# Performance work log

Hardware: AMD Instinct MI355X
Metric: run time of the kernel (lower is better)

Reference implementation:

```python
import jax, jax.numpy as jnp
import numpy as np
import math

N, E = 50000, 800000
DM, H, L = 128, 8, 6
D = DM // H  # per-head dim = 16
FF = 4 * DM
EPS = 1e-5


def _ln(x, g, b):
    mu = jnp.mean(x, axis=-1, keepdims=True)
    var = jnp.mean((x - mu) ** 2, axis=-1, keepdims=True)
    return (x - mu) * jax.lax.rsqrt(var + EPS) * g + b


def setup_inputs() -> dict:
    key = jax.random.key(0)
    ks = jax.random.split(key, 20)
    s = 0.05
    inp = {
        "node_features": jax.random.normal(ks[0], (N, 20), jnp.float32),
        "edge_attr": jax.random.normal(ks[1], (E, 3), jnp.float32),
        "edge_index": jax.random.randint(ks[2], (2, E), 0, N, jnp.int32),
        "emb_W": jax.random.normal(ks[3], (20, DM), jnp.float32) * s,
        "emb_b": jnp.zeros((DM,), jnp.float32),
        "Wq": jax.random.normal(ks[4], (L, DM, DM), jnp.float32) * s,
        "Wk": jax.random.normal(ks[5], (L, DM, DM), jnp.float32) * s,
        "Wv": jax.random.normal(ks[6], (L, DM, DM), jnp.float32) * s,
        "eW1": jax.random.normal(ks[7], (L, 3, D), jnp.float32) * s,
        "eb1": jnp.zeros((L, D), jnp.float32),
        "eW2": jax.random.normal(ks[8], (L, D, DM), jnp.float32) * s,
        "eb2": jnp.zeros((L, DM), jnp.float32),
        "ln_g": jnp.ones((L, DM), jnp.float32),
        "ln_b": jnp.zeros((L, DM), jnp.float32),
        "ff_W1": jax.random.normal(ks[9], (L, DM, FF), jnp.float32) * s,
        "ff_b1": jnp.zeros((L, FF), jnp.float32),
        "ff_W2": jax.random.normal(ks[10], (L, FF, DM), jnp.float32) * s,
        "ff_b2": jnp.zeros((L, DM), jnp.float32),
    }
    return inp


def reference(node_features, edge_attr, emb_W, emb_b, Wq, Wk, Wv,
              eW1, eb1, eW2, eb2, ln_g, ln_b, ff_W1, ff_b1, ff_W2, ff_b2,
              edge_index):
    src = edge_index[0]  # j: message source
    dst = edge_index[1]  # i: message target
    x = node_features @ emb_W + emb_b  # [N, DM]
    scale = 1.0 / math.sqrt(D)
    for l in range(L):
        q = (x @ Wq[l]).reshape(N, H, D)
        k = (x @ Wk[l]).reshape(N, H, D)
        v = (x @ Wv[l]).reshape(N, H, D)
        ee = (jnp.maximum(edge_attr @ eW1[l] + eb1[l], 0.0) @ eW2[l] + eb2[l]).reshape(E, H, D)
        # per-edge attention logits over heads (softmax over head axis, as in source)
        attn = jnp.einsum('ehd,ehd->eh', q[dst], k[src] + ee) * scale
        attn = jax.nn.softmax(attn, axis=1)  # [E, H]
        msg = (attn[..., None] * v[src]).reshape(E, H * D)  # per-head messages, concat heads
        agg = jax.ops.segment_sum(msg, dst, num_segments=N)  # scatter-add
        x = _ln(x + agg, ln_g[l], ln_b[l])
        h = jnp.maximum(x @ ff_W1[l] + ff_b1[l], 0.0) @ ff_W2[l] + ff_b2[l]
        x = _ln(x + h, ln_g[l], ln_b[l])  # same LN params reused, as in source
    return x
```

## Files before the change

kernel.cpp:

```cpp
#include <hip/hip_runtime.h>
#include <cstdint>
#include <cstddef>

#define NN 50000
#define NE 800000
#define NP 50048
#define ROWT 391

typedef unsigned short u16;
typedef _Float16 f16;
typedef _Float16 hf8 __attribute__((ext_vector_type(8)));
typedef float f32x4 __attribute__((ext_vector_type(4)));

union U32 { unsigned u; f16 h[2]; };
union U64 { uint2 v; f16 h[4]; };
union U128 { uint4 v; f16 x[8]; };

__device__ __forceinline__ float b2f(u16 v){ return __uint_as_float((unsigned)v << 16); }
__device__ __forceinline__ u16 f2b(float f){
  unsigned u = __float_as_uint(f);
  return (u16)((u + 0x7fffu + ((u >> 16) & 1u)) >> 16);
}
__device__ __forceinline__ float ldf(const void* p, long i, int f32){
  return f32 ? ((const float*)p)[i] : b2f(((const u16*)p)[i]);
}
__device__ __forceinline__ void gl_lds16(const void* g, void* l){
  __builtin_amdgcn_global_load_lds((const __attribute__((address_space(1))) void*)g,
                                   (__attribute__((address_space(3))) void*)l, 16, 0, 0);
}

__global__ void detect_k(const u16* __restrict__ nf, int* __restrict__ flag)
{
  int mx = 0;
  for (int i = 0; i < 256; ++i) { int e = (nf[i] >> 7) & 0xFF; mx = e > mx ? e : mx; }
  flag[0] = (mx >= 0x90) ? 1 : 0;
}

__global__ void zero_i_k(int* __restrict__ p, int n)
{
  int i = blockIdx.x * 256 + threadIdx.x;
  if (i < n) p[i] = 0;
}

__global__ void conv_k(const void* eW1, const void* eb1, const void* eb2,
                       const void* lng, const void* lnb, const void* fb1, const void* fb2,
                       const void* embB, const void* embW,
                       float* __restrict__ pf, const int* __restrict__ dflag)
{
  int f32 = dflag[0];
  int i = blockIdx.x * 256 + threadIdx.x;
  if (i >= 9216) return;
  const void* p; long off;
  if (i < 288)       { p = eW1;  off = i; }
  else if (i < 384)  { p = eb1;  off = i - 288; }
  else if (i < 1152) { p = eb2;  off = i - 384; }
  else if (i < 1920) { p = lng;  off = i - 1152; }
  else if (i < 2688) { p = lnb;  off = i - 1920; }
  else if (i < 5760) { p = fb1;  off = i - 2688; }
  else if (i < 6528) { p = fb2;  off = i - 5760; }
  else if (i < 6656) { p = embB; off = i - 6528; }
  else               { p = embW; off = i - 6656; }
  pf[i] = ldf(p, off, f32);
}

__global__ void prep_qkve_k(const void* __restrict__ Wq, const void* __restrict__ Wk,
                            const void* __restrict__ Wv, const void* __restrict__ eW2,
                            f16* __restrict__ Wcat, const int* __restrict__ dflag)
{
  int f32 = dflag[0];
  int idx = blockIdx.x * 256 + threadIdx.x;
  int l = idx >> 16;
  int rem = idx & 65535;
  int r = rem >> 7;
  int kk = rem & 127;
  long base = (long)l * 16384;
  float val;
  if (r < 384) {
    const void* W = (r < 128) ? Wq : (r < 256) ? Wk : Wv;
    int n = r & 127;
    val = ldf(W, base + kk * 128 + n, f32);
  } else {
    int n = r - 384, h = n >> 4, j = n & 15;
    long wq = base + kk * 128 + h * 16;
    long e2 = (long)l * 2048 + j * 128 + h * 16;
    float s = 0.f;
    #pragma unroll
    for (int d = 0; d < 16; ++d) s += ldf(Wq, wq + d, f32) * ldf(eW2, e2 + d, f32);
    val = s;
  }
  Wcat[idx] = (f16)val;
}

__global__ void transpose_k(const void* __restrict__ in, f16* __restrict__ out, int R, int C,
                            const int* __restrict__ dflag)
{
  int f32 = dflag[0];
  int idx = blockIdx.x * 256 + threadIdx.x;
  int rc = R * C;
  int l = idx / rc, rem = idx % rc;
  int r = rem / C, c = rem % C;
  out[l * rc + c * R + r] = (f16)ldf(in, idx, f32);
}

__global__ void deg_count_k(const int* __restrict__ eidx, int* __restrict__ deg)
{
  int e = blockIdx.x * 256 + threadIdx.x;
  if (e < NE) atomicAdd(&deg[eidx[NE + e]], 1);
}

__global__ void scan_k(const int* __restrict__ deg, int* __restrict__ rstart,
                       int* __restrict__ cursor, int Nn)
{
  __shared__ int sums[1024];
  int t = threadIdx.x;
  int chunk = (Nn + 1023) >> 10;
  int start = t * chunk;
  int end = start + chunk; if (end > Nn) end = Nn;
  int s = 0;
  for (int i = start; i < end; ++i) s += deg[i];
  sums[t] = s;
  __syncthreads();
  for (int o = 1; o < 1024; o <<= 1) {
    int v = (t >= o) ? sums[t - o] : 0;
    __syncthreads();
    sums[t] += v;
    __syncthreads();
  }
  int run = (t == 0) ? 0 : sums[t - 1];
  for (int i = start; i < end; ++i) { rstart[i] = run; cursor[i] = run; run += deg[i]; }
  if (end == Nn && start < Nn) rstart[Nn] = run;
}

__global__ void csr_fill_k(const int* __restrict__ eidx, int* __restrict__ cursor,
                           int* __restrict__ csrc, int* __restrict__ cdst,
                           int* __restrict__ ceid)
{
  int e = blockIdx.x * 256 + threadIdx.x;
  if (e >= NE) return;
  int d = eidx[NE + e];
  int slot = atomicAdd(&cursor[d], 1);
  csrc[slot] = eidx[e];
  cdst[slot] = d;
  ceid[slot] = e;
}

__global__ void ea_gather_k(const void* __restrict__ eatt, const int* __restrict__ ceid,
                            f16* __restrict__ ea4, const int* __restrict__ dflag)
{
  int f32 = dflag[0];
  int e = blockIdx.x * 256 + threadIdx.x;
  if (e >= NE) return;
  long id = ceid[e];
  f16* q = ea4 + (size_t)e * 4;
  q[0] = (f16)ldf(eatt, id * 3 + 0, f32);
  q[1] = (f16)ldf(eatt, id * 3 + 1, f32);
  q[2] = (f16)ldf(eatt, id * 3 + 2, f32);
  q[3] = (f16)0.f;
}

__global__ void emb_k(const void* __restrict__ nf, const float* __restrict__ embWf,
                      const float* __restrict__ embBf, float* __restrict__ xf,
                      f16* __restrict__ xh, const int* __restrict__ dflag)
{
  int f32 = dflag[0];
  int idx = blockIdx.x * 256 + threadIdx.x;
  int node = idx >> 7, c = idx & 127;
  float s = 0.f;
  if (node < NN) {
    s = embBf[c];
    long row = (long)node * 20;
    #pragma unroll
    for (int f = 0; f < 20; ++f) s += ldf(nf, row + f, f32) * embWf[f * 128 + c];
  }
  xf[idx] = s;
  xh[idx] = (f16)s;
}

template<int MODE>
__global__ __launch_bounds__(256)
void gemm_k(const f16* __restrict__ A, const f16* __restrict__ Bt, int K,
            f16* __restrict__ o0, f16* __restrict__ o1, f16* __restrict__ o3,
            const float* __restrict__ bias)
{
  __shared__ __align__(16) f16 lA[128 * 32];
  __shared__ __align__(16) f16 lB[128 * 32];
  const int tid = threadIdx.x;
  const int wave = tid >> 6, lane = tid & 63;
  const int wr = wave >> 1, wc = wave & 1;
  const size_t rowBase = (size_t)blockIdx.x * 128;
  const size_t colBase = (size_t)blockIdx.y * 128;
  const int m = lane & 15, q4 = lane >> 4;

  f32x4 zero = {0.f, 0.f, 0.f, 0.f};
  f32x4 acc[4][4];
  #pragma unroll
  for (int i = 0; i < 4; ++i)
    #pragma unroll
    for (int j = 0; j < 4; ++j) acc[i][j] = zero;

  const int lr = lane >> 2, lq = lane & 3;
  const f16* Ap = A + (rowBase + wave * 32 + lr) * (size_t)K + lq * 8;
  const f16* Bp = Bt + (colBase + wave * 32 + lr) * (size_t)K + lq * 8;
  f16* lAp = lA + wave * 1024;
  f16* lBp = lB + wave * 1024;

  for (int k0 = 0; k0 < K; k0 += 32) {
    gl_lds16(Ap + k0, lAp);
    gl_lds16(Ap + k0 + (size_t)16 * K, lAp + 512);
    gl_lds16(Bp + k0, lBp);
    gl_lds16(Bp + k0 + (size_t)16 * K, lBp + 512);
    __syncthreads();
    hf8 af[4], bf[4];
    #pragma unroll
    for (int i = 0; i < 4; ++i) af[i] = *(const hf8*)(lA + (wr * 64 + i * 16 + m) * 32 + q4 * 8);
    #pragma unroll
    for (int j = 0; j < 4; ++j) bf[j] = *(const hf8*)(lB + (wc * 64 + j * 16 + m) * 32 + q4 * 8);
    #pragma unroll
    for (int i = 0; i < 4; ++i)
      #pragma unroll
      for (int j = 0; j < 4; ++j)
        acc[i][j] = __builtin_amdgcn_mfma_f32_16x16x32_f16(af[i], bf[j], acc[i][j], 0, 0, 0);
    __syncthreads();
  }

  if (MODE == 0) {
    f16* o; size_t ld; int off;
    if (blockIdx.y == 0)      { o = o0; ld = 128; off = 0; }
    else if (blockIdx.y == 1) { o = o1; ld = 256; off = 0; }
    else if (blockIdx.y == 2) { o = o1; ld = 256; off = 128; }
    else                      { o = o3; ld = 128; off = 0; }
    #pragma unroll
    for (int i = 0; i < 4; ++i)
      #pragma unroll
      for (int r = 0; r < 4; ++r) {
        size_t row = rowBase + wr * 64 + i * 16 + q4 * 4 + r;
        #pragma unroll
        for (int j = 0; j < 4; ++j) {
          int col = wc * 64 + j * 16 + m;
          o[row * ld + off + col] = (f16)acc[i][j][r];
        }
      }
  } else if (MODE == 1) {
    #pragma unroll
    for (int j = 0; j < 4; ++j) {
      int colg = (int)colBase + wc * 64 + j * 16 + m;
      float bv = bias[colg];
      #pragma unroll
      for (int i = 0; i < 4; ++i)
        #pragma unroll
        for (int r = 0; r < 4; ++r) {
          size_t row = rowBase + wr * 64 + i * 16 + q4 * 4 + r;
          o0[row * 512 + colg] = (f16)fmaxf(acc[i][j][r] + bv, 0.f);
        }
    }
  } else {
    #pragma unroll
    for (int j = 0; j < 4; ++j) {
      int colg = wc * 64 + j * 16 + m;
      float bv = bias[colg];
      #pragma unroll
      for (int i = 0; i < 4; ++i)
        #pragma unroll
        for (int r = 0; r < 4; ++r) {
          size_t row = rowBase + wr * 64 + i * 16 + q4 * 4 + r;
          o0[row * 128 + colg] = (f16)(acc[i][j][r] + bv);
        }
    }
  }
}

__global__ void pb_k(const f16* __restrict__ qf, const float* __restrict__ eb2f,
                     float* __restrict__ pbt)
{
  int idx = blockIdx.x * 256 + threadIdx.x;
  if (idx >= NN * 8) return;
  int n = idx >> 3, h = idx & 7;
  U128 a, b;
  a.v = *(const uint4*)(qf + (size_t)n * 128 + h * 16);
  b.v = *(const uint4*)(qf + (size_t)n * 128 + h * 16 + 8);
  const float* e = eb2f + h * 16;
  float p = 0.f;
  #pragma unroll
  for (int d = 0; d < 8; ++d) p = fmaf((float)a.x[d], e[d], fmaf((float)b.x[d], e[8 + d], p));
  pbt[idx] = p;
}

__global__ __launch_bounds__(256)
void attn_k(const f16* __restrict__ qf, const f16* __restrict__ kv, const f16* __restrict__ qef,
            const f16* __restrict__ ea4, const int* __restrict__ csrc, const int* __restrict__ cdst,
            const float* __restrict__ pbt, const float* __restrict__ eW1f,
            const float* __restrict__ eb1f, f16* __restrict__ w8)
{
  int e = blockIdx.x * 256 + threadIdx.x;
  if (e >= NE) return;
  int src = csrc[e], dst = cdst[e];
  U64 ue; ue.v = *(const uint2*)(ea4 + (size_t)e * 4);
  float a0 = (float)ue.h[0], a1 = (float)ue.h[1], a2 = (float)ue.h[2];
  float he[16];
  #pragma unroll
  for (int j = 0; j < 16; ++j)
    he[j] = fmaxf(fmaf(a2, eW1f[32 + j], fmaf(a1, eW1f[16 + j], fmaf(a0, eW1f[j], eb1f[j]))), 0.f);
  const uint4* qr = (const uint4*)(qf + (size_t)dst * 128);
  const uint4* kr = (const uint4*)(kv + (size_t)src * 256);
  const uint4* er = (const uint4*)(qef + (size_t)dst * 128);
  float4 pb0 = *(const float4*)(pbt + (size_t)dst * 8);
  float4 pb1 = *(const float4*)(pbt + (size_t)dst * 8 + 4);
  float pbv[8] = { pb0.x, pb0.y, pb0.z, pb0.w, pb1.x, pb1.y, pb1.z, pb1.w };
  float logit[8];
  uint4 qa = qr[0], qb = qr[1], ka = kr[0], kb = kr[1], za = er[0], zb = er[1];
  #pragma unroll
  for (int h = 0; h < 8; ++h) {
    uint4 qa2, qb2, ka2, kb2, za2, zb2;
    if (h < 7) {
      qa2 = qr[2*h+2]; qb2 = qr[2*h+3];
      ka2 = kr[2*h+2]; kb2 = kr[2*h+3];
      za2 = er[2*h+2]; zb2 = er[2*h+3];
    }
    U128 Q0, Q1, K0, K1, E0, E1;
    Q0.v = qa; Q1.v = qb; K0.v = ka; K1.v = kb; E0.v = za; E1.v = zb;
    float p = 0.f;
    #pragma unroll
    for (int d = 0; d < 8; ++d) {
      p = fmaf((float)Q0.x[d], (float)K0.x[d], p);
      p = fmaf((float)Q1.x[d], (float)K1.x[d], p);
      p = fmaf((float)E0.x[d], he[d], p);
      p = fmaf((float)E1.x[d], he[8 + d], p);
    }
    logit[h] = (p + pbv[h]) * 0.25f;
    qa = qa2; qb = qb2; ka = ka2; kb = kb2; za = za2; zb = zb2;
  }
  float mx = logit[0];
  #pragma unroll
  for (int h = 1; h < 8; ++h) mx = fmaxf(mx, logit[h]);
  float se = 0.f, ex[8];
  #pragma unroll
  for (int h = 0; h < 8; ++h) { ex[h] = __expf(logit[h] - mx); se += ex[h]; }
  float inv = 1.f / se;
  U128 W;
  #pragma unroll
  for (int h = 0; h < 8; ++h) W.x[h] = (f16)(ex[h] * inv);
  *(uint4*)(w8 + (size_t)e * 8) = W.v;
}

__global__ void agg_k(const f16* __restrict__ kv, const f16* __restrict__ w8,
                      const int* __restrict__ rstart, const int* __restrict__ csrc,
                      const float* __restrict__ gf, const float* __restrict__ bpf,
                      float* __restrict__ xf, f16* __restrict__ xh)
{
  int wave = threadIdx.x >> 6, lane = threadIdx.x & 63;
  int node = blockIdx.x * 4 + wave;
  if (node >= NN) return;
  int sub = lane >> 4, l = lane & 15;
  int c0 = l << 3;
  int head = l >> 1;
  float acc[8] = {0.f, 0.f, 0.f, 0.f, 0.f, 0.f, 0.f, 0.f};
  int e0 = rstart[node], e1 = rstart[node + 1];
  int e = e0 + sub;
  uint4 vN = {0, 0, 0, 0}; float wN = 0.f;
  if (e < e1) {
    int s = csrc[e];
    vN = *(const uint4*)(kv + (size_t)s * 256 + 128 + c0);
    wN = (float)w8[(size_t)e * 8 + head];
  }
  for (; e < e1; e += 4) {
    uint4 vC = vN; float wC = wN;
    int en = e + 4;
    if (en < e1) {
      int s = csrc[en];
      vN = *(const uint4*)(kv + (size_t)s * 256 + 128 + c0);
      wN = (float)w8[(size_t)en * 8 + head];
    }
    U128 V; V.v = vC;
    #pragma unroll
    for (int i = 0; i < 8; ++i) acc[i] = fmaf(wC, (float)V.x[i], acc[i]);
  }
  #pragma unroll
  for (int i = 0; i < 8; ++i) {
    acc[i] += __shfl_xor(acc[i], 16);
    acc[i] += __shfl_xor(acc[i], 32);
  }
  size_t nb = (size_t)node * 128 + c0;
  float4 x0 = *(const float4*)(xf + nb);
  float4 x1 = *(const float4*)(xf + nb + 4);
  float y[8] = { x0.x + acc[0], x0.y + acc[1], x0.z + acc[2], x0.w + acc[3],
                 x1.x + acc[4], x1.y + acc[5], x1.z + acc[6], x1.w + acc[7] };
  float s1 = 0.f, s2 = 0.f;
  #pragma unroll
  for (int i = 0; i < 8; ++i) { s1 += y[i]; s2 += y[i] * y[i]; }
  #pragma unroll
  for (int o = 1; o < 16; o <<= 1) { s1 += __shfl_xor(s1, o); s2 += __shfl_xor(s2, o); }
  float mu = s1 * 0.0078125f;
  float var = s2 * 0.0078125f - mu * mu;
  float rstd = rsqrtf(var + 1e-5f);
  float ov[8];
  #pragma unroll
  for (int i = 0; i < 8; ++i) ov[i] = (y[i] - mu) * rstd * gf[c0 + i] + bpf[c0 + i];
  if (sub == 0) {
    float4 s0 = { ov[0], ov[1], ov[2], ov[3] };
    float4 s1v = { ov[4], ov[5], ov[6], ov[7] };
    *(float4*)(xf + nb) = s0;
    *(float4*)(xf + nb + 4) = s1v;
    U128 wz;
    #pragma unroll
    for (int i = 0; i < 8; ++i) wz.x[i] = (f16)ov[i];
    *(uint4*)(xh + nb) = wz.v;
  }
}

__global__ void ln_res_k(const f16* __restrict__ add, float* __restrict__ xf,
                         f16* __restrict__ xh, const float* __restrict__ gf,
                         const float* __restrict__ bpf)
{
  int wave = threadIdx.x >> 6, lane = threadIdx.x & 63;
  int node = blockIdx.x * 4 + wave;
  if (node >= NN) return;
  int c0 = lane << 1;
  size_t nb = (size_t)node * 128 + c0;
  U32 ua; ua.u = *(const unsigned*)(add + nb);
  float y0 = xf[nb] + (float)ua.h[0];
  float y1 = xf[nb + 1] + (float)ua.h[1];
  float s1 = y0 + y1, s2 = y0 * y0 + y1 * y1;
  #pragma unroll
  for (int o = 1; o < 64; o <<= 1) { s1 += __shfl_xor(s1, o); s2 += __shfl_xor(s2, o); }
  float mu = s1 * 0.0078125f;
  float var = s2 * 0.0078125f - mu * mu;
  float rstd = rsqrtf(var + 1e-5f);
  float o0v = (y0 - mu) * rstd * gf[c0] + bpf[c0];
  float o1v = (y1 - mu) * rstd * gf[c0 + 1] + bpf[c0 + 1];
  xf[nb] = o0v; xf[nb + 1] = o1v;
  U32 wz; wz.h[0] = (f16)o0v; wz.h[1] = (f16)o1v;
  *(unsigned*)(xh + nb) = wz.u;
}

__global__ void out_k(const float* __restrict__ xf, void* __restrict__ out,
                      const int* __restrict__ dflag)
{
  int f32 = dflag[0];
  int idx = blockIdx.x * 256 + threadIdx.x;
  if (f32) ((float*)out)[idx] = xf[idx];
  else     ((u16*)out)[idx] = f2b(xf[idx]);
}

extern "C" void kernel_launch(void* const* d_in, const int* in_sizes, int n_in,
                              void* d_out, int out_size, void* d_ws, size_t ws_size,
                              hipStream_t stream)
{
  const void* nf   = d_in[0];
  const void* eatt = d_in[1];
  const int*  eidx = (const int*)d_in[2];
  const void* embW = d_in[3];
  const void* embB = d_in[4];
  const void* Wq   = d_in[5];
  const void* Wk   = d_in[6];
  const void* Wv   = d_in[7];
  const void* eW1  = d_in[8];
  const void* eb1  = d_in[9];
  const void* eW2  = d_in[10];
  const void* eb2  = d_in[11];
  const void* lng  = d_in[12];
  const void* lnb  = d_in[13];
  const void* fW1  = d_in[14];
  const void* fb1  = d_in[15];
  const void* fW2  = d_in[16];
  const void* fb2  = d_in[17];

  char* p = (char*)d_ws;
  auto alloc = [&](size_t b) { char* r = p; p += (b + 255) & ~(size_t)255; return r; };
  int* dflag   = (int*)alloc(256);
  float* pf    = (float*)alloc(9216 * 4);
  float* xf    = (float*)alloc((size_t)NP * 128 * 4);
  f16*   xh    = (f16*)  alloc((size_t)NP * 128 * 2);
  int* deg     = (int*)alloc((NN + 1) * 4);
  int* rst     = (int*)alloc((NN + 1) * 4);
  int* cur     = (int*)alloc((size_t)NN * 4);
  int* csrc    = (int*)alloc((size_t)NE * 4);
  int* cdst    = (int*)alloc((size_t)NE * 4);
  float* pbt   = (float*)alloc((size_t)NN * 8 * 4);
  f16* ea4     = (f16*)alloc((size_t)NE * 4 * 2);
  f16* Wcat    = (f16*)alloc((size_t)6 * 512 * 128 * 2);
  f16* W1t     = (f16*)alloc((size_t)6 * 512 * 128 * 2);
  f16* W2t     = (f16*)alloc((size_t)6 * 128 * 512 * 2);
  char* S    = alloc((size_t)NP * 512 * 2 + (size_t)NP * 128 * 2);
  f16* qf  = (f16*)S;
  f16* qe  = qf + (size_t)NP * 128;
  f16* kv  = qe + (size_t)NP * 128;
  f16* hb  = (f16*)S;
  f16* ffh = hb + (size_t)NP * 512;
  f16* w8  = ffh;
  int* ceid = (int*)S;

  float* eW1f = pf;
  float* eb1f = pf + 288;
  float* eb2f = pf + 384;
  float* lngf = pf + 1152;
  float* lnbf = pf + 1920;
  float* fb1f = pf + 2688;
  float* fb2f = pf + 5760;
  float* embBf = pf + 6528;
  float* embWf = pf + 6656;

  detect_k<<<1, 1, 0, stream>>>((const u16*)nf, dflag);
  conv_k<<<36, 256, 0, stream>>>(eW1, eb1, eb2, lng, lnb, fb1, fb2, embB, embW, pf, dflag);
  prep_qkve_k<<<1536, 256, 0, stream>>>(Wq, Wk, Wv, eW2, Wcat, dflag);
  transpose_k<<<1536, 256, 0, stream>>>(fW1, W1t, 128, 512, dflag);
  transpose_k<<<1536, 256, 0, stream>>>(fW2, W2t, 512, 128, dflag);
  zero_i_k<<<(NN + 256) / 256, 256, 0, stream>>>(deg, NN + 1);
  deg_count_k<<<3125, 256, 0, stream>>>(eidx, deg);
  scan_k<<<1, 1024, 0, stream>>>(deg, rst, cur, NN);
  csr_fill_k<<<3125, 256, 0, stream>>>(eidx, cur, csrc, cdst, ceid);
  ea_gather_k<<<3125, 256, 0, stream>>>(eatt, ceid, ea4, dflag);
  emb_k<<<NP * 128 / 256, 256, 0, stream>>>(nf, embWf, embBf, xf, xh, dflag);

  for (int l = 0; l < 6; ++l) {
    gemm_k<0><<<dim3(ROWT, 4), 256, 0, stream>>>(xh, Wcat + (size_t)l * 65536, 128,
                                                 qf, kv, qe, nullptr);
    pb_k<<<(NN * 8 + 255) / 256, 256, 0, stream>>>(qf, eb2f + l * 128, pbt);
    attn_k<<<3125, 256, 0, stream>>>(qf, kv, qe, ea4, csrc, cdst, pbt,
                                     eW1f + l * 48, eb1f + l * 16, w8);
    agg_k<<<12500, 256, 0, stream>>>(kv, w8, rst, csrc,
                                     lngf + l * 128, lnbf + l * 128, xf, xh);
    gemm_k<1><<<dim3(ROWT, 4), 256, 0, stream>>>(xh, W1t + (size_t)l * 65536, 128,
                                                 hb, nullptr, nullptr, fb1f + l * 512);
    gemm_k<2><<<dim3(ROWT, 1), 256, 0, stream>>>(hb, W2t + (size_t)l * 65536, 512,
                                                 ffh, nullptr, nullptr, fb2f + l * 128);
    ln_res_k<<<12500, 256, 0, stream>>>(ffh, xf, xh, lngf + l * 128, lnbf + l * 128);
  }
  out_k<<<25000, 256, 0, stream>>>(xf, d_out, dflag);
}
```

Before: 1.517 ms.

## Parallelize degree prefix scan across blocks and deepen GEMM K-tile to 64

```diff
diff --git a/kernel.cpp b/kernel.cpp
--- a/kernel.cpp
+++ b/kernel.cpp
@@ -6,6 +6,7 @@
 #define NE 800000
 #define NP 50048
 #define ROWT 391
+#define NBLK 196
 
 typedef unsigned short u16;
 typedef _Float16 f16;
@@ -108,27 +109,48 @@
   if (e < NE) atomicAdd(&deg[eidx[NE + e]], 1);
 }
 
-__global__ void scan_k(const int* __restrict__ deg, int* __restrict__ rstart,
-                       int* __restrict__ cursor, int Nn)
-{
-  __shared__ int sums[1024];
+__global__ void scan_a(const int* __restrict__ deg, int* __restrict__ bsum)
+{
+  __shared__ int tmp[256];
+  int t = threadIdx.x, i = blockIdx.x * 256 + t;
+  int v = (i < NN) ? deg[i] : 0;
+  tmp[t] = v; __syncthreads();
+  for (int o = 1; o < 256; o <<= 1) {
+    int u = (t >= o) ? tmp[t - o] : 0;
+    __syncthreads(); tmp[t] += u; __syncthreads();
+  }
+  if (t == 255) bsum[blockIdx.x] = tmp[255];
+}
+
+__global__ void scan_b(const int* __restrict__ bsum, int* __restrict__ boff)
+{
+  __shared__ int tmp[256];
   int t = threadIdx.x;
-  int chunk = (Nn + 1023) >> 10;
-  int start = t * chunk;
-  int end = start + chunk; if (end > Nn) end = Nn;
-  int s = 0;
-  for (int i = start; i < end; ++i) s += deg[i];
-  sums[t] = s;
-  __syncthreads();
-  for (int o = 1; o < 1024; o <<= 1) {
-    int v = (t >= o) ? sums[t - o] : 0;
-    __syncthreads();
-    sums[t] += v;
-    __syncthreads();
-  }
-  int run = (t == 0) ? 0 : sums[t - 1];
-  for (int i = start; i < end; ++i) { rstart[i] = run; cursor[i] = run; run += deg[i]; }
-  if (end == Nn && start < Nn) rstart[Nn] = run;
+  int v = (t < NBLK) ? bsum[t] : 0;
+  tmp[t] = v; __syncthreads();
+  for (int o = 1; o < 256; o <<= 1) {
+    int u = (t >= o) ? tmp[t - o] : 0;
+    __syncthreads(); tmp[t] += u; __syncthreads();
+  }
+  if (t < NBLK) boff[t] = tmp[t] - v;
+}
+
+__global__ void scan_c(const int* __restrict__ deg, const int* __restrict__ boff,
+                       int* __restrict__ rstart, int* __restrict__ cursor)
+{
+  __shared__ int tmp[256];
+  int t = threadIdx.x, i = blockIdx.x * 256 + t;
+  int v = (i < NN) ? deg[i] : 0;
+  tmp[t] = v; __syncthreads();
+  for (int o = 1; o < 256; o <<= 1) {
+    int u = (t >= o) ? tmp[t - o] : 0;
+    __syncthreads(); tmp[t] += u; __syncthreads();
+  }
+  if (i <= NN) {
+    int ex = boff[blockIdx.x] + tmp[t] - v;
+    rstart[i] = ex;
+    if (i < NN) cursor[i] = ex;
+  }
 }
 
 __global__ void csr_fill_k(const int* __restrict__ eidx, int* __restrict__ cursor,
@@ -182,8 +204,8 @@
             f16* __restrict__ o0, f16* __restrict__ o1, f16* __restrict__ o3,
             const float* __restrict__ bias)
 {
-  __shared__ __align__(16) f16 lA[128 * 32];
-  __shared__ __align__(16) f16 lB[128 * 32];
+  __shared__ __align__(16) f16 lA[128 * 64];
+  __shared__ __align__(16) f16 lB[128 * 64];
   const int tid = threadIdx.x;
   const int wave = tid >> 6, lane = tid & 63;
   const int wr = wave >> 1, wc = wave & 1;
@@ -198,28 +220,34 @@
     #pragma unroll
     for (int j = 0; j < 4; ++j) acc[i][j] = zero;
 
-  const int lr = lane >> 2, lq = lane & 3;
-  const f16* Ap = A + (rowBase + wave * 32 + lr) * (size_t)K + lq * 8;
-  const f16* Bp = Bt + (colBase + wave * 32 + lr) * (size_t)K + lq * 8;
-  f16* lAp = lA + wave * 1024;
-  f16* lBp = lB + wave * 1024;
-
-  for (int k0 = 0; k0 < K; k0 += 32) {
-    gl_lds16(Ap + k0, lAp);
-    gl_lds16(Ap + k0 + (size_t)16 * K, lAp + 512);
-    gl_lds16(Bp + k0, lBp);
-    gl_lds16(Bp + k0 + (size_t)16 * K, lBp + 512);
+  const int sr = lane >> 3, sc = lane & 7;
+  const f16* Ap = A + (rowBase + wave * 32 + sr) * (size_t)K + sc * 8;
+  const f16* Bp = Bt + (colBase + wave * 32 + sr) * (size_t)K + sc * 8;
+  f16* lAp = lA + wave * 2048;
+  f16* lBp = lB + wave * 2048;
+
+  for (int k0 = 0; k0 < K; k0 += 64) {
+    #pragma unroll
+    for (int i = 0; i < 4; ++i) {
+      gl_lds16(Ap + k0 + (size_t)(8 * i) * K, lAp + i * 512);
+      gl_lds16(Bp + k0 + (size_t)(8 * i) * K, lBp + i * 512);
+    }
     __syncthreads();
-    hf8 af[4], bf[4];
-    #pragma unroll
-    for (int i = 0; i < 4; ++i) af[i] = *(const hf8*)(lA + (wr * 64 + i * 16 + m) * 32 + q4 * 8);
-    #pragma unroll
-    for (int j = 0; j < 4; ++j) bf[j] = *(const hf8*)(lB + (wc * 64 + j * 16 + m) * 32 + q4 * 8);
-    #pragma unroll
-    for (int i = 0; i < 4; ++i)
+    hf8 af[2][4], bf[2][4];
+    #pragma unroll
+    for (int s = 0; s < 2; ++s)
       #pragma unroll
-      for (int j = 0; j < 4; ++j)
-        acc[i][j] = __builtin_amdgcn_mfma_f32_16x16x32_f16(af[i], bf[j], acc[i][j], 0, 0, 0);
+      for (int i = 0; i < 4; ++i) {
+        af[s][i] = *(const hf8*)(lA + (wr * 64 + i * 16 + m) * 64 + s * 32 + q4 * 8);
+        bf[s][i] = *(const hf8*)(lB + (wc * 64 + i * 16 + m) * 64 + s * 32 + q4 * 8);
+      }
+    #pragma unroll
+    for (int s = 0; s < 2; ++s)
+      #pragma unroll
+      for (int i = 0; i < 4; ++i)
+        #pragma unroll
+        for (int j = 0; j < 4; ++j)
+          acc[i][j] = __builtin_amdgcn_mfma_f32_16x16x32_f16(af[s][i], bf[s][j], acc[i][j], 0, 0, 0);
     __syncthreads();
   }
 
@@ -473,6 +501,8 @@
   int* deg     = (int*)alloc((NN + 1) * 4);
   int* rst     = (int*)alloc((NN + 1) * 4);
   int* cur     = (int*)alloc((size_t)NN * 4);
+  int* bsum    = (int*)alloc(NBLK * 4);
+  int* boff    = (int*)alloc(NBLK * 4);
   int* csrc    = (int*)alloc((size_t)NE * 4);
   int* cdst    = (int*)alloc((size_t)NE * 4);
   float* pbt   = (float*)alloc((size_t)NN * 8 * 4);
@@ -506,7 +536,9 @@
   transpose_k<<<1536, 256, 0, stream>>>(fW2, W2t, 512, 128, dflag);
   zero_i_k<<<(NN + 256) / 256, 256, 0, stream>>>(deg, NN + 1);
   deg_count_k<<<3125, 256, 0, stream>>>(eidx, deg);
-  scan_k<<<1, 1024, 0, stream>>>(deg, rst, cur, NN);
+  scan_a<<<NBLK, 256, 0, stream>>>(deg, bsum);
+  scan_b<<<1, 256, 0, stream>>>(bsum, boff);
+  scan_c<<<NBLK, 256, 0, stream>>>(deg, boff, rst, cur);
   csr_fill_k<<<3125, 256, 0, stream>>>(eidx, cur, csrc, cdst, ceid);
   ea_gather_k<<<3125, 256, 0, stream>>>(eatt, ceid, ea4, dflag);
   emb_k<<<NP * 128 / 256, 256, 0, stream>>>(nf, embWf, embBf, xf, xh, dflag);
```

New measurement: 1.406 ms. 7.3% less time.
